# Performance work log

Measured on AMD Instinct MI355X. Metric: run time of the kernel, lower is better.

The kernel has to match this reference:

```python
import jax, jax.numpy as jnp
import numpy as np


def setup_inputs() -> dict:
    key = jax.random.key(0)
    k0, k1, k2, k3, k4 = jax.random.split(key, 5)
    B, N, H, d, kproj = 4, 2048, 8, 32, 256
    queries = jax.random.normal(k0, (B, N, H, d), dtype=jnp.float32)
    keys = jax.random.normal(k1, (B, N, H, d), dtype=jnp.float32)
    values = jax.random.normal(k2, (B, N, H, d), dtype=jnp.float32)
    # Linformer sequence projections [N, k]; scaled so projected K/V keep unit-ish variance
    E_proj = jax.random.normal(k3, (N, kproj), dtype=jnp.float32) * 0.02
    F_proj = jax.random.normal(k4, (N, kproj), dtype=jnp.float32) * 0.02
    return {"queries": queries, "keys": keys, "values": values,
            "E_proj": E_proj, "F_proj": F_proj}


def reference(queries, keys, values, E_proj, F_proj):
    """Hybrid attention of dsfa_former:
      (1) FullAttention with triangular causal mask (manual einsum+softmax)
      (2) LinearAttentionHead: Linformer-style sequence projection of K/V via E/F.
    Dropout is identity (eval). Returns (out_full, out_lin), each [B, N, H, d].
    """
    B, N, H, d = queries.shape
    scale = 1.0 / jnp.sqrt(jnp.asarray(d, queries.dtype))

    # ---- FullAttention (causal) ----
    scores = jnp.einsum('blhe,bshe->bhls', queries, keys)  # [B,H,N,N]
    causal = jnp.triu(jnp.ones((N, N), dtype=bool), k=1)   # True above diag -> masked
    scores = jnp.where(causal, -jnp.inf, scores)
    A = jax.nn.softmax(scale * scores, axis=-1)
    out_full = jnp.einsum('bhls,bshd->blhd', A, values)    # [B,N,H,d]

    # ---- LinearAttentionHead (Linformer, no causal mask since kp != N) ----
    Qb = queries.transpose(0, 2, 1, 3)  # [B,H,N,d]
    Kb = keys.transpose(0, 2, 1, 3)
    Vb = values.transpose(0, 2, 1, 3)
    Kp = jnp.einsum('bhnd,nk->bhkd', Kb, E_proj)           # [B,H,k,d]
    Vp = jnp.einsum('bhnd,nk->bhkd', Vb, F_proj)           # [B,H,k,d]
    s_lin = jnp.einsum('bhnd,bhkd->bhnk', Qb, Kp) * scale  # d_k == d
    P = jax.nn.softmax(s_lin, axis=-1)
    out_lin = jnp.einsum('bhnk,bhkd->bhnd', P, Vp).transpose(0, 2, 1, 3)  # [B,N,H,d]

    return out_full, out_lin
```

## Files before the change

kernel.cpp:

```cpp
#include <hip/hip_runtime.h>
#include <hip/hip_bf16.h>


typedef __bf16 bf16x8 __attribute__((ext_vector_type(8)));
typedef __bf16 bf16x2 __attribute__((ext_vector_type(2)));
typedef float f32x4 __attribute__((ext_vector_type(4)));

union BF8 { uint4 u4; ushort us[8]; bf16x8 b; unsigned u32[4]; };

constexpr int B_ = 4, N_ = 2048, H_ = 8, D_ = 32, KP_ = 256, BH_ = 32;
constexpr float SCL2 = 0.25505654442633533f;
constexpr int NFULL = 1024;
constexpr int CHK = 32 * D_;

__device__ __forceinline__ ushort f2bf(float f) {
  unsigned u = __builtin_bit_cast(unsigned, f);
  return (ushort)((u + 0x7FFFu + ((u >> 16) & 1u)) >> 16);
}
__device__ __forceinline__ unsigned pkbf(float f0, float f1) {
#if __has_builtin(__builtin_amdgcn_cvt_pk_bf16_f32)
  bf16x2 r = __builtin_amdgcn_cvt_pk_bf16_f32(f0, f1);
  return __builtin_bit_cast(unsigned, r);
#else
  unsigned u0 = __builtin_bit_cast(unsigned, f0) + 0x8000u;
  unsigned u1 = __builtin_bit_cast(unsigned, f1) + 0x8000u;
  return __builtin_amdgcn_perm(u1, u0, 0x07060302);
#endif
}
__device__ __forceinline__ float bflo(unsigned u) {
  return __builtin_bit_cast(float, u << 16);
}
__device__ __forceinline__ float bfhi(unsigned u) {
  return __builtin_bit_cast(float, u & 0xFFFF0000u);
}

__device__ __forceinline__ void load8_bf(const float* __restrict__ p,
                                         float scale, BF8& hi) {
  float4 a = *reinterpret_cast<const float4*>(p);
  float4 b = *reinterpret_cast<const float4*>(p + 4);
  float x[8] = {a.x, a.y, a.z, a.w, b.x, b.y, b.z, b.w};
#pragma unroll
  for (int i = 0; i < 8; ++i) hi.us[i] = f2bf(x[i] * scale);
}

__global__ __launch_bounds__(256) void k_prep(const float* __restrict__ K,
                                              const float* __restrict__ V,
                                              const float* __restrict__ E,
                                              const float* __restrict__ F,
                                              ushort* __restrict__ KH,
                                              ushort* __restrict__ Kt,
                                              ushort* __restrict__ Vt,
                                              ushort* __restrict__ Et,
                                              ushort* __restrict__ Ft) {
  __shared__ alignas(16) ushort S[4224];
  const int idx = blockIdx.x;
  const int t = threadIdx.x;
  if (idx < 1024) {
    ushort* Tk = S;
    ushort* Tv = S + 2112;
    const int bh = idx >> 5, b = bh >> 3, h = bh & 7;
    const int n0 = (idx & 31) * 64;
    {
      const int row = t >> 2, e8 = (t & 3) * 8;
      const size_t gbase = ((size_t)(b * N_ + n0 + row) * H_ + h) * D_ + e8;
      float4 k0 = *reinterpret_cast<const float4*>(K + gbase);
      float4 k1 = *reinterpret_cast<const float4*>(K + gbase + 4);
      float4 v0 = *reinterpret_cast<const float4*>(V + gbase);
      float4 v1 = *reinterpret_cast<const float4*>(V + gbase + 4);
      float kk[8] = {k0.x,k0.y,k0.z,k0.w,k1.x,k1.y,k1.z,k1.w};
      float vv[8] = {v0.x,v0.y,v0.z,v0.w,v1.x,v1.y,v1.z,v1.w};
      BF8 xh;
#pragma unroll
      for (int i = 0; i < 8; ++i) {
        xh.us[i] = f2bf(kk[i]);
        Tk[(e8 + i) * 66 + row] = xh.us[i];
        Tv[(e8 + i) * 66 + row] = f2bf(vv[i]);
      }
      *reinterpret_cast<uint4*>(KH + ((size_t)bh * N_ + n0 + row) * D_ + e8) = xh.u4;
    }
    __syncthreads();
    {
      const int e = t >> 3, n8 = (t & 7) * 8;
      BF8 xk, xv;
#pragma unroll
      for (int i = 0; i < 8; ++i) {
        xk.us[i] = Tk[e * 66 + n8 + i];
        xv.us[i] = Tv[e * 66 + n8 + i];
      }
      const size_t ob = ((size_t)bh * D_ + e) * N_ + n0 + n8;
      *reinterpret_cast<uint4*>(Kt + ob) = xk.u4;
      *reinterpret_cast<uint4*>(Vt + ob) = xv.u4;
    }
  } else {
    const int j = idx - 1024;
    const float* src = (j >> 7) ? F : E;
    ushort* dst = (j >> 7) ? Ft : Et;
    const int jj = j & 127;
    const int n0 = (jj & 31) * 64, kp0 = (jj >> 5) * 64;
    ushort* T = S;
    {
      const int n = t >> 2, c16 = (t & 3) * 16;
      const size_t gbase = (size_t)(n0 + n) * KP_ + kp0 + c16;
#pragma unroll
      for (int q = 0; q < 4; ++q) {
        float4 x = *reinterpret_cast<const float4*>(src + gbase + q * 4);
        T[(c16 + q * 4 + 0) * 66 + n] = f2bf(x.x);
        T[(c16 + q * 4 + 1) * 66 + n] = f2bf(x.y);
        T[(c16 + q * 4 + 2) * 66 + n] = f2bf(x.z);
        T[(c16 + q * 4 + 3) * 66 + n] = f2bf(x.w);
      }
    }
    __syncthreads();
    {
      const int kp = t >> 2, n16 = (t & 3) * 16;
      BF8 x0, x1;
#pragma unroll
      for (int i = 0; i < 8; ++i) {
        x0.us[i] = T[kp * 66 + n16 + i];
        x1.us[i] = T[kp * 66 + n16 + 8 + i];
      }
      const size_t ob = (size_t)(kp0 + kp) * N_ + n0 + n16;
      *reinterpret_cast<uint4*>(dst + ob) = x0.u4;
      *reinterpret_cast<uint4*>(dst + ob + 8) = x1.u4;
    }
  }
}

__global__ __launch_bounds__(256) void k_linproj(const ushort* __restrict__ Et,
                                                 const ushort* __restrict__ Ft,
                                                 const ushort* __restrict__ Kt,
                                                 const ushort* __restrict__ Vt,
                                                 ushort* __restrict__ Kp,
                                                 ushort* __restrict__ Vpt) {
  __shared__ float L[4][64][16];
  const int bh = blockIdx.y;
  const int t = threadIdx.x;
  const int w = t >> 6, lane = t & 63, quad = lane >> 4, l15 = lane & 15;
  const int kp16 = blockIdx.x * 16;
  const int nbase = w * (N_ / 4);

  const ushort* eA = Et + (size_t)(kp16 + l15) * N_ + nbase + quad * 8;
  const ushort* fA = Ft + (size_t)(kp16 + l15) * N_ + nbase + quad * 8;
  const ushort* kB0 = Kt + ((size_t)bh * D_ + l15) * N_ + nbase + quad * 8;
  const ushort* kB1 = kB0 + (size_t)16 * N_;
  const ushort* vB0 = Vt + ((size_t)bh * D_ + l15) * N_ + nbase + quad * 8;
  const ushort* vB1 = vB0 + (size_t)16 * N_;

  f32x4 accK0 = {0.f,0.f,0.f,0.f}, accK1 = {0.f,0.f,0.f,0.f};
  f32x4 accV0 = {0.f,0.f,0.f,0.f}, accV1 = {0.f,0.f,0.f,0.f};

  for (int n0 = 0; n0 < N_ / 4; n0 += 32) {
    BF8 aE, aF, b0, b1, b2, b3;
    aE.u4 = *reinterpret_cast<const uint4*>(eA + n0);
    aF.u4 = *reinterpret_cast<const uint4*>(fA + n0);
    b0.u4 = *reinterpret_cast<const uint4*>(kB0 + n0);
    b1.u4 = *reinterpret_cast<const uint4*>(kB1 + n0);
    b2.u4 = *reinterpret_cast<const uint4*>(vB0 + n0);
    b3.u4 = *reinterpret_cast<const uint4*>(vB1 + n0);
    accK0 = __builtin_amdgcn_mfma_f32_16x16x32_bf16(aE.b, b0.b, accK0, 0, 0, 0);
    accK1 = __builtin_amdgcn_mfma_f32_16x16x32_bf16(aE.b, b1.b, accK1, 0, 0, 0);
    accV0 = __builtin_amdgcn_mfma_f32_16x16x32_bf16(aF.b, b2.b, accV0, 0, 0, 0);
    accV1 = __builtin_amdgcn_mfma_f32_16x16x32_bf16(aF.b, b3.b, accV1, 0, 0, 0);
  }

#pragma unroll
  for (int r = 0; r < 4; ++r) {
    L[w][lane][r]      = accK0[r];
    L[w][lane][4 + r]  = accK1[r];
    L[w][lane][8 + r]  = accV0[r];
    L[w][lane][12 + r] = accV1[r];
  }
  __syncthreads();
#pragma unroll
  for (int r = 0; r < 4; ++r) {
    const float v = L[0][lane][w * 4 + r] + L[1][lane][w * 4 + r] +
                    L[2][lane][w * 4 + r] + L[3][lane][w * 4 + r];
    const int kp = kp16 + quad * 4 + r;
    if (w == 0)      Kp[((size_t)bh * KP_ + kp) * D_ + l15]       = f2bf(v);
    else if (w == 1) Kp[((size_t)bh * KP_ + kp) * D_ + 16 + l15]  = f2bf(v);
    else if (w == 2) Vpt[((size_t)bh * D_ + l15) * KP_ + kp]      = f2bf(v);
    else             Vpt[((size_t)bh * D_ + 16 + l15) * KP_ + kp] = f2bf(v);
  }
}

__global__ __launch_bounds__(256) void k_attn(const float* __restrict__ Q,
                                              const ushort* __restrict__ KH,
                                              const ushort* __restrict__ Vt,
                                              const ushort* __restrict__ Kp,
                                              const ushort* __restrict__ Vpt,
                                              float* __restrict__ out) {
  __shared__ unsigned Op[4][4][64][5];
  const int idx = blockIdx.x;
  const int t = threadIdx.x;
  const int w = t >> 6, lane = t & 63;
  const int quad = lane >> 4, l15 = lane & 15;
  const int kperm1 = 8 * (l15 >> 2) + (l15 & 3);
  const f32x4 z = {0.f,0.f,0.f,0.f};

  if (idx < NFULL) {
    const int bh = (idx & 7) + 8 * ((idx >> 3) & 3);
    const int m = 31 - (idx >> 5);
    const int b = bh >> 3, h = bh & 7;
    const int q0 = 64 * m;

    BF8 qh[4];
#pragma unroll
    for (int tt = 0; tt < 4; ++tt)
      load8_bf(Q + ((size_t)(b * N_ + q0 + 16 * tt + l15) * H_ + h) * D_ + quad * 8,
               SCL2, qh[tt]);

    const ushort* KHl = KH + (size_t)bh * N_ * D_ + (size_t)kperm1 * D_ + quad * 8;
    const ushort* V0l = Vt + ((size_t)bh * D_ + l15) * N_ + quad * 8;
    const ushort* V1l = V0l + (size_t)16 * N_;

    const int nun = 2 * m;
    const int cb = (w * nun) >> 2;
    const int ce = ((w + 1) * nun) >> 2;
    const int nwu = ce - cb;

    f32x4 O0[4], O1[4];
    float ls[4];
#pragma unroll
    for (int tt = 0; tt < 4; ++tt) { O0[tt] = z; O1[tt] = z; ls[tt] = 0.f; }

    BF8 kA1, kA2, vA0, vA1, kB1, kB2, vB0, vB1;

    auto procU = [&](BF8& k1, BF8& k2, BF8& v0, BF8& v1) {
#pragma unroll
      for (int tt = 0; tt < 4; ++tt) {
        f32x4 s1 = __builtin_amdgcn_mfma_f32_16x16x32_bf16(k1.b, qh[tt].b, z, 0, 0, 0);
        f32x4 s2 = __builtin_amdgcn_mfma_f32_16x16x32_bf16(k2.b, qh[tt].b, z, 0, 0, 0);
        float e0 = exp2f(s1[0]), e1 = exp2f(s1[1]), e2 = exp2f(s1[2]), e3 = exp2f(s1[3]);
        float e4 = exp2f(s2[0]), e5 = exp2f(s2[1]), e6 = exp2f(s2[2]), e7 = exp2f(s2[3]);
        ls[tt] += ((e0 + e1) + (e2 + e3)) + ((e4 + e5) + (e6 + e7));
        BF8 p;
        p.u32[0] = pkbf(e0, e1); p.u32[1] = pkbf(e2, e3);
        p.u32[2] = pkbf(e4, e5); p.u32[3] = pkbf(e6, e7);
        O0[tt] = __builtin_amdgcn_mfma_f32_16x16x32_bf16(p.b, v0.b, O0[tt], 0, 0, 0);
        O1[tt] = __builtin_amdgcn_mfma_f32_16x16x32_bf16(p.b, v1.b, O1[tt], 0, 0, 0);
      }
    };
    auto procM = [&](BF8& k1, BF8& k2, BF8& v0, BF8& v1, int ta, bool doUnm) {
#pragma unroll
      for (int d = 0; d < 2; ++d) {
        const int tt = ta + d;
        const int thr = d ? 16 + l15 : l15;
        f32x4 s1 = __builtin_amdgcn_mfma_f32_16x16x32_bf16(k1.b, qh[tt].b, z, 0, 0, 0);
        f32x4 s2 = __builtin_amdgcn_mfma_f32_16x16x32_bf16(k2.b, qh[tt].b, z, 0, 0, 0);
        float e[8];
#pragma unroll
        for (int j = 0; j < 8; ++j) {
          const float sv = (j < 4) ? s1[j] : s2[j - 4];
          e[j] = (8 * quad + j <= thr) ? exp2f(sv) : 0.f;
        }
        ls[tt] += ((e[0] + e[1]) + (e[2] + e[3])) + ((e[4] + e[5]) + (e[6] + e[7]));
        BF8 p;
        p.u32[0] = pkbf(e[0], e[1]); p.u32[1] = pkbf(e[2], e[3]);
        p.u32[2] = pkbf(e[4], e[5]); p.u32[3] = pkbf(e[6], e[7]);
        O0[tt] = __builtin_amdgcn_mfma_f32_16x16x32_bf16(p.b, v0.b, O0[tt], 0, 0, 0);
        O1[tt] = __builtin_amdgcn_mfma_f32_16x16x32_bf16(p.b, v1.b, O1[tt], 0, 0, 0);
      }
      if (doUnm) {
#pragma unroll
        for (int tt = 2; tt < 4; ++tt) {
          f32x4 s1 = __builtin_amdgcn_mfma_f32_16x16x32_bf16(k1.b, qh[tt].b, z, 0, 0, 0);
          f32x4 s2 = __builtin_amdgcn_mfma_f32_16x16x32_bf16(k2.b, qh[tt].b, z, 0, 0, 0);
          float e0 = exp2f(s1[0]), e1 = exp2f(s1[1]), e2 = exp2f(s1[2]), e3 = exp2f(s1[3]);
          float e4 = exp2f(s2[0]), e5 = exp2f(s2[1]), e6 = exp2f(s2[2]), e7 = exp2f(s2[3]);
          ls[tt] += ((e0 + e1) + (e2 + e3)) + ((e4 + e5) + (e6 + e7));
          BF8 p;
          p.u32[0] = pkbf(e0, e1); p.u32[1] = pkbf(e2, e3);
          p.u32[2] = pkbf(e4, e5); p.u32[3] = pkbf(e6, e7);
          O0[tt] = __builtin_amdgcn_mfma_f32_16x16x32_bf16(p.b, v0.b, O0[tt], 0, 0, 0);
          O1[tt] = __builtin_amdgcn_mfma_f32_16x16x32_bf16(p.b, v1.b, O1[tt], 0, 0, 0);
        }
      }
    };

    kA1.u4 = *reinterpret_cast<const uint4*>(KHl + (size_t)cb * CHK);
    kA2.u4 = *reinterpret_cast<const uint4*>(KHl + (size_t)cb * CHK + 4 * D_);
    vA0.u4 = *reinterpret_cast<const uint4*>(V0l + cb * 32);
    vA1.u4 = *reinterpret_cast<const uint4*>(V1l + cb * 32);
    kB1.u4 = *reinterpret_cast<const uint4*>(KHl + (size_t)(cb + 1) * CHK);
    kB2.u4 = *reinterpret_cast<const uint4*>(KHl + (size_t)(cb + 1) * CHK + 4 * D_);
    vB0.u4 = *reinterpret_cast<const uint4*>(V0l + (cb + 1) * 32);
    vB1.u4 = *reinterpret_cast<const uint4*>(V1l + (cb + 1) * 32);

    const ushort* pKA = KHl + (size_t)(cb + 2) * CHK;
    const ushort* pKB = KHl + (size_t)(cb + 3) * CHK;
    const ushort* pV0 = V0l + (cb + 2) * 32;
    const ushort* pV1 = V1l + (cb + 2) * 32;

    int i = 0;
    for (; i + 2 <= nwu; i += 2) {
      procU(kA1, kA2, vA0, vA1);
      kA1.u4 = *reinterpret_cast<const uint4*>(pKA);
      kA2.u4 = *reinterpret_cast<const uint4*>(pKA + 4 * D_);
      vA0.u4 = *reinterpret_cast<const uint4*>(pV0);
      vA1.u4 = *reinterpret_cast<const uint4*>(pV1);
      procU(kB1, kB2, vB0, vB1);
      kB1.u4 = *reinterpret_cast<const uint4*>(pKB);
      kB2.u4 = *reinterpret_cast<const uint4*>(pKB + 4 * D_);
      vB0.u4 = *reinterpret_cast<const uint4*>(pV0 + 32);
      vB1.u4 = *reinterpret_cast<const uint4*>(pV1 + 32);
      pKA += 2 * CHK; pKB += 2 * CHK; pV0 += 64; pV1 += 64;
    }
    if (i < nwu) {
      procU(kA1, kA2, vA0, vA1);
      if (w == 3) procM(kB1, kB2, vB0, vB1, 0, true);
    } else if (w == 3) {
      procM(kA1, kA2, vA0, vA1, 0, true);
    }
    if (w == 2) {
      const int c2 = nun + 1;
      kB1.u4 = *reinterpret_cast<const uint4*>(KHl + (size_t)c2 * CHK);
      kB2.u4 = *reinterpret_cast<const uint4*>(KHl + (size_t)c2 * CHK + 4 * D_);
      vB0.u4 = *reinterpret_cast<const uint4*>(V0l + c2 * 32);
      vB1.u4 = *reinterpret_cast<const uint4*>(V1l + c2 * 32);
      procM(kB1, kB2, vB0, vB1, 2, false);
    }

#pragma unroll
    for (int tt = 0; tt < 4; ++tt) {
      Op[w][tt][lane][0] = pkbf(O0[tt][0], O0[tt][1]);
      Op[w][tt][lane][1] = pkbf(O0[tt][2], O0[tt][3]);
      Op[w][tt][lane][2] = pkbf(O1[tt][0], O1[tt][1]);
      Op[w][tt][lane][3] = pkbf(O1[tt][2], O1[tt][3]);
      Op[w][tt][lane][4] = __builtin_bit_cast(unsigned, ls[tt]);
    }
    __syncthreads();
    {
      const int tt = w;
      float l = __builtin_bit_cast(float, Op[0][tt][lane][4]) +
                __builtin_bit_cast(float, Op[1][tt][lane][4]) +
                __builtin_bit_cast(float, Op[2][tt][lane][4]) +
                __builtin_bit_cast(float, Op[3][tt][lane][4]);
      l += __shfl_xor(l, 16);
      l += __shfl_xor(l, 32);
      const float inv = __builtin_amdgcn_rcpf(l);
      float A0[4] = {0.f,0.f,0.f,0.f}, A1[4] = {0.f,0.f,0.f,0.f};
#pragma unroll
      for (int s = 0; s < 4; ++s) {
        const unsigned u0 = Op[s][tt][lane][0], u1 = Op[s][tt][lane][1];
        const unsigned u2 = Op[s][tt][lane][2], u3 = Op[s][tt][lane][3];
        A0[0] += bflo(u0); A0[1] += bfhi(u0);
        A0[2] += bflo(u1); A0[3] += bfhi(u1);
        A1[0] += bflo(u2); A1[1] += bfhi(u2);
        A1[2] += bflo(u3); A1[3] += bfhi(u3);
      }
#pragma unroll
      for (int r = 0; r < 4; ++r) {
        const float fr = __shfl(inv, quad * 4 + r, 16);
        const int q = q0 + 16 * tt + quad * 4 + r;
        const size_t base = ((size_t)(b * N_ + q) * H_ + h) * D_;
        out[base + l15]      = A0[r] * fr;
        out[base + 16 + l15] = A1[r] * fr;
      }
    }
  } else {
    const int j = idx - NFULL;
    const int bh = (j & 7) + 8 * ((j >> 3) & 3);
    const int b = bh >> 3, h = bh & 7;
    const int q0 = (j >> 5) * 64 + w * 16;
    float* olin = out + (size_t)B_ * N_ * H_ * D_;

    BF8 qh;
    load8_bf(Q + ((size_t)(b * N_ + q0 + l15) * H_ + h) * D_ + quad * 8, SCL2, qh);

    const int kperm2 = kperm1 + 4;
    const ushort* KpHb = Kp + (size_t)bh * KP_ * D_ + quad * 8;
    const ushort* Vp0 = Vpt + ((size_t)bh * D_ + l15) * KP_ + quad * 8;
    const ushort* Vp1 = Vp0 + (size_t)16 * KP_;

    f32x4 s1[8], s2[8];
    float sum = 0.f;
#pragma unroll
    for (int g = 0; g < 8; ++g) {
      const int kp0 = g * 32;
      BF8 a1, a2;
      a1.u4 = *reinterpret_cast<const uint4*>(KpHb + (size_t)(kp0 + kperm1) * D_);
      a2.u4 = *reinterpret_cast<const uint4*>(KpHb + (size_t)(kp0 + kperm2) * D_);
      s1[g] = __builtin_amdgcn_mfma_f32_16x16x32_bf16(a1.b, qh.b, z, 0, 0, 0);
      s2[g] = __builtin_amdgcn_mfma_f32_16x16x32_bf16(a2.b, qh.b, z, 0, 0, 0);
#pragma unroll
      for (int r = 0; r < 4; ++r) {
        s1[g][r] = exp2f(s1[g][r]);
        s2[g][r] = exp2f(s2[g][r]);
        sum += s1[g][r] + s2[g][r];
      }
    }
    sum += __shfl_xor(sum, 16);
    sum += __shfl_xor(sum, 32);
    const float inv = __builtin_amdgcn_rcpf(sum);

    f32x4 O0 = z, O1 = z;
#pragma unroll
    for (int g = 0; g < 8; ++g) {
      BF8 p;
      p.u32[0] = pkbf(s1[g][0] * inv, s1[g][1] * inv);
      p.u32[1] = pkbf(s1[g][2] * inv, s1[g][3] * inv);
      p.u32[2] = pkbf(s2[g][0] * inv, s2[g][1] * inv);
      p.u32[3] = pkbf(s2[g][2] * inv, s2[g][3] * inv);
      BF8 v0, v1;
      v0.u4 = *reinterpret_cast<const uint4*>(Vp0 + g * 32);
      v1.u4 = *reinterpret_cast<const uint4*>(Vp1 + g * 32);
      O0 = __builtin_amdgcn_mfma_f32_16x16x32_bf16(p.b, v0.b, O0, 0, 0, 0);
      O1 = __builtin_amdgcn_mfma_f32_16x16x32_bf16(p.b, v1.b, O1, 0, 0, 0);
    }

#pragma unroll
    for (int r = 0; r < 4; ++r) {
      const int q = q0 + quad * 4 + r;
      const size_t base = ((size_t)(b * N_ + q) * H_ + h) * D_;
      olin[base + l15]      = O0[r];
      olin[base + 16 + l15] = O1[r];
    }
  }
}

extern "C" void kernel_launch(void* const* d_in, const int* in_sizes, int n_in,
                              void* d_out, int out_size, void* d_ws, size_t ws_size,
                              hipStream_t stream) {
  const float* Q = (const float*)d_in[0];
  const float* K = (const float*)d_in[1];
  const float* V = (const float*)d_in[2];
  const float* E = (const float*)d_in[3];
  const float* F = (const float*)d_in[4];
  float* out = (float*)d_out;

  ushort* KH  = (ushort*)d_ws;
  ushort* Kt  = KH + (size_t)BH_ * N_ * D_;
  ushort* Vt  = Kt + (size_t)BH_ * N_ * D_;
  ushort* Et  = Vt + (size_t)BH_ * N_ * D_;
  ushort* Ft  = Et + (size_t)KP_ * N_;
  ushort* Kp  = Ft + (size_t)KP_ * N_;
  ushort* Vpt = Kp + (size_t)BH_ * KP_ * D_;

  k_prep<<<dim3(1280), 256, 0, stream>>>(K, V, E, F, KH, Kt, Vt, Et, Ft);
  k_linproj<<<dim3(KP_ / 16, BH_), 256, 0, stream>>>(Et, Ft, Kt, Vt, Kp, Vpt);
  k_attn<<<dim3(NFULL + 1024), 256, 0, stream>>>(Q, KH, Vt, Kp, Vpt, out);
}
```

Measured before the change: 146.4 us.

## Compute softmax row sums via MFMA with ones vector and use raw exp2

Replaces per-lane VALU accumulation of exponentials with an extra MFMA against an all-ones bf16 operand, so row sums come out in the output layout and the shuffle reductions go away. Uses the hardware exp2 intrinsic instead of exp2f, adds an occupancy hint to launch bounds, and packs the shared-memory partial outputs into 16-byte vector stores with a separate small row-sum buffer. In the Linformer branch, normalisation moves after the PV product so unnormalised probabilities are packed once. This adds MFMA work per tile, and the row sums are now built from bf16-rounded probabilities.

```diff
diff --git a/kernel.cpp b/kernel.cpp
--- a/kernel.cpp
+++ b/kernel.cpp
@@ -32,6 +32,13 @@
 }
 __device__ __forceinline__ float bfhi(unsigned u) {
   return __builtin_bit_cast(float, u & 0xFFFF0000u);
+}
+__device__ __forceinline__ float ex2(float x) {
+#if __has_builtin(__builtin_amdgcn_exp2f)
+  return __builtin_amdgcn_exp2f(x);
+#else
+  return exp2f(x);
+#endif
 }
 
 __device__ __forceinline__ void load8_bf(const float* __restrict__ p,
@@ -183,13 +190,14 @@
   }
 }
 
-__global__ __launch_bounds__(256) void k_attn(const float* __restrict__ Q,
-                                              const ushort* __restrict__ KH,
-                                              const ushort* __restrict__ Vt,
-                                              const ushort* __restrict__ Kp,
-                                              const ushort* __restrict__ Vpt,
-                                              float* __restrict__ out) {
-  __shared__ unsigned Op[4][4][64][5];
+__global__ __launch_bounds__(256, 4) void k_attn(const float* __restrict__ Q,
+                                                 const ushort* __restrict__ KH,
+                                                 const ushort* __restrict__ Vt,
+                                                 const ushort* __restrict__ Kp,
+                                                 const ushort* __restrict__ Vpt,
+                                                 float* __restrict__ out) {
+  __shared__ alignas(16) unsigned Op[4][4][64][4];
+  __shared__ float Ls[4][4][4][4];
   const int idx = blockIdx.x;
   const int t = threadIdx.x;
   const int w = t >> 6, lane = t & 63;
@@ -197,6 +205,10 @@
   const int kperm1 = 8 * (l15 >> 2) + (l15 & 3);
   const f32x4 z = {0.f,0.f,0.f,0.f};
 
+  BF8 ones;
+#pragma unroll
+  for (int i2 = 0; i2 < 4; ++i2) ones.u32[i2] = 0x3F803F80u;
+
   if (idx < NFULL) {
     const int bh = (idx & 7) + 8 * ((idx >> 3) & 3);
     const int m = 31 - (idx >> 5);
@@ -218,10 +230,9 @@
     const int ce = ((w + 1) * nun) >> 2;
     const int nwu = ce - cb;
 
-    f32x4 O0[4], O1[4];
-    float ls[4];
-#pragma unroll
-    for (int tt = 0; tt < 4; ++tt) { O0[tt] = z; O1[tt] = z; ls[tt] = 0.f; }
+    f32x4 O0[4], O1[4], LS[4];
+#pragma unroll
+    for (int tt = 0; tt < 4; ++tt) { O0[tt] = z; O1[tt] = z; LS[tt] = z; }
 
     BF8 kA1, kA2, vA0, vA1, kB1, kB2, vB0, vB1;
 
@@ -230,14 +241,14 @@
       for (int tt = 0; tt < 4; ++tt) {
         f32x4 s1 = __builtin_amdgcn_mfma_f32_16x16x32_bf16(k1.b, qh[tt].b, z, 0, 0, 0);
         f32x4 s2 = __builtin_amdgcn_mfma_f32_16x16x32_bf16(k2.b, qh[tt].b, z, 0, 0, 0);
-        float e0 = exp2f(s1[0]), e1 = exp2f(s1[1]), e2 = exp2f(s1[2]), e3 = exp2f(s1[3]);
-        float e4 = exp2f(s2[0]), e5 = exp2f(s2[1]), e6 = exp2f(s2[2]), e7 = exp2f(s2[3]);
-        ls[tt] += ((e0 + e1) + (e2 + e3)) + ((e4 + e5) + (e6 + e7));
+        float e0 = ex2(s1[0]), e1 = ex2(s1[1]), e2 = ex2(s1[2]), e3 = ex2(s1[3]);
+        float e4 = ex2(s2[0]), e5 = ex2(s2[1]), e6 = ex2(s2[2]), e7 = ex2(s2[3]);
         BF8 p;
         p.u32[0] = pkbf(e0, e1); p.u32[1] = pkbf(e2, e3);
         p.u32[2] = pkbf(e4, e5); p.u32[3] = pkbf(e6, e7);
         O0[tt] = __builtin_amdgcn_mfma_f32_16x16x32_bf16(p.b, v0.b, O0[tt], 0, 0, 0);
         O1[tt] = __builtin_amdgcn_mfma_f32_16x16x32_bf16(p.b, v1.b, O1[tt], 0, 0, 0);
+        LS[tt] = __builtin_amdgcn_mfma_f32_16x16x32_bf16(p.b, ones.b, LS[tt], 0, 0, 0);
       }
     };
     auto procM = [&](BF8& k1, BF8& k2, BF8& v0, BF8& v1, int ta, bool doUnm) {
@@ -251,28 +262,28 @@
 #pragma unroll
         for (int j = 0; j < 8; ++j) {
           const float sv = (j < 4) ? s1[j] : s2[j - 4];
-          e[j] = (8 * quad + j <= thr) ? exp2f(sv) : 0.f;
+          e[j] = (8 * quad + j <= thr) ? ex2(sv) : 0.f;
         }
-        ls[tt] += ((e[0] + e[1]) + (e[2] + e[3])) + ((e[4] + e[5]) + (e[6] + e[7]));
         BF8 p;
         p.u32[0] = pkbf(e[0], e[1]); p.u32[1] = pkbf(e[2], e[3]);
         p.u32[2] = pkbf(e[4], e[5]); p.u32[3] = pkbf(e[6], e[7]);
         O0[tt] = __builtin_amdgcn_mfma_f32_16x16x32_bf16(p.b, v0.b, O0[tt], 0, 0, 0);
         O1[tt] = __builtin_amdgcn_mfma_f32_16x16x32_bf16(p.b, v1.b, O1[tt], 0, 0, 0);
+        LS[tt] = __builtin_amdgcn_mfma_f32_16x16x32_bf16(p.b, ones.b, LS[tt], 0, 0, 0);
       }
       if (doUnm) {
 #pragma unroll
         for (int tt = 2; tt < 4; ++tt) {
           f32x4 s1 = __builtin_amdgcn_mfma_f32_16x16x32_bf16(k1.b, qh[tt].b, z, 0, 0, 0);
           f32x4 s2 = __builtin_amdgcn_mfma_f32_16x16x32_bf16(k2.b, qh[tt].b, z, 0, 0, 0);
-          float e0 = exp2f(s1[0]), e1 = exp2f(s1[1]), e2 = exp2f(s1[2]), e3 = exp2f(s1[3]);
-          float e4 = exp2f(s2[0]), e5 = exp2f(s2[1]), e6 = exp2f(s2[2]), e7 = exp2f(s2[3]);
-          ls[tt] += ((e0 + e1) + (e2 + e3)) + ((e4 + e5) + (e6 + e7));
+          float e0 = ex2(s1[0]), e1 = ex2(s1[1]), e2 = ex2(s1[2]), e3 = ex2(s1[3]);
+          float e4 = ex2(s2[0]), e5 = ex2(s2[1]), e6 = ex2(s2[2]), e7 = ex2(s2[3]);
           BF8 p;
           p.u32[0] = pkbf(e0, e1); p.u32[1] = pkbf(e2, e3);
           p.u32[2] = pkbf(e4, e5); p.u32[3] = pkbf(e6, e7);
           O0[tt] = __builtin_amdgcn_mfma_f32_16x16x32_bf16(p.b, v0.b, O0[tt], 0, 0, 0);
           O1[tt] = __builtin_amdgcn_mfma_f32_16x16x32_bf16(p.b, v1.b, O1[tt], 0, 0, 0);
+          LS[tt] = __builtin_amdgcn_mfma_f32_16x16x32_bf16(p.b, ones.b, LS[tt], 0, 0, 0);
         }
       }
     };
@@ -322,39 +333,44 @@
 
 #pragma unroll
     for (int tt = 0; tt < 4; ++tt) {
-      Op[w][tt][lane][0] = pkbf(O0[tt][0], O0[tt][1]);
-      Op[w][tt][lane][1] = pkbf(O0[tt][2], O0[tt][3]);
-      Op[w][tt][lane][2] = pkbf(O1[tt][0], O1[tt][1]);
-      Op[w][tt][lane][3] = pkbf(O1[tt][2], O1[tt][3]);
-      Op[w][tt][lane][4] = __builtin_bit_cast(unsigned, ls[tt]);
+      uint4 pk;
+      pk.x = pkbf(O0[tt][0], O0[tt][1]);
+      pk.y = pkbf(O0[tt][2], O0[tt][3]);
+      pk.z = pkbf(O1[tt][0], O1[tt][1]);
+      pk.w = pkbf(O1[tt][2], O1[tt][3]);
+      *reinterpret_cast<uint4*>(Op[w][tt][lane]) = pk;
+    }
+    if (l15 == 0) {
+#pragma unroll
+      for (int tt = 0; tt < 4; ++tt)
+#pragma unroll
+        for (int r = 0; r < 4; ++r) Ls[w][tt][quad][r] = LS[tt][r];
     }
     __syncthreads();
     {
       const int tt = w;
-      float l = __builtin_bit_cast(float, Op[0][tt][lane][4]) +
-                __builtin_bit_cast(float, Op[1][tt][lane][4]) +
-                __builtin_bit_cast(float, Op[2][tt][lane][4]) +
-                __builtin_bit_cast(float, Op[3][tt][lane][4]);
-      l += __shfl_xor(l, 16);
-      l += __shfl_xor(l, 32);
-      const float inv = __builtin_amdgcn_rcpf(l);
+      float iv[4];
+#pragma unroll
+      for (int r = 0; r < 4; ++r) {
+        const float l = Ls[0][tt][quad][r] + Ls[1][tt][quad][r] +
+                        Ls[2][tt][quad][r] + Ls[3][tt][quad][r];
+        iv[r] = __builtin_amdgcn_rcpf(l);
+      }
       float A0[4] = {0.f,0.f,0.f,0.f}, A1[4] = {0.f,0.f,0.f,0.f};
 #pragma unroll
       for (int s = 0; s < 4; ++s) {
-        const unsigned u0 = Op[s][tt][lane][0], u1 = Op[s][tt][lane][1];
-        const unsigned u2 = Op[s][tt][lane][2], u3 = Op[s][tt][lane][3];
-        A0[0] += bflo(u0); A0[1] += bfhi(u0);
-        A0[2] += bflo(u1); A0[3] += bfhi(u1);
-        A1[0] += bflo(u2); A1[1] += bfhi(u2);
-        A1[2] += bflo(u3); A1[3] += bfhi(u3);
+        const uint4 u = *reinterpret_cast<const uint4*>(Op[s][tt][lane]);
+        A0[0] += bflo(u.x); A0[1] += bfhi(u.x);
+        A0[2] += bflo(u.y); A0[3] += bfhi(u.y);
+        A1[0] += bflo(u.z); A1[1] += bfhi(u.z);
+        A1[2] += bflo(u.w); A1[3] += bfhi(u.w);
       }
 #pragma unroll
       for (int r = 0; r < 4; ++r) {
-        const float fr = __shfl(inv, quad * 4 + r, 16);
         const int q = q0 + 16 * tt + quad * 4 + r;
         const size_t base = ((size_t)(b * N_ + q) * H_ + h) * D_;
-        out[base + l15]      = A0[r] * fr;
-        out[base + 16 + l15] = A1[r] * fr;
+        out[base + l15]      = A0[r] * iv[r];
+        out[base + 16 + l15] = A1[r] * iv[r];
       }
     }
   } else {
@@ -372,48 +388,40 @@
     const ushort* Vp0 = Vpt + ((size_t)bh * D_ + l15) * KP_ + quad * 8;
     const ushort* Vp1 = Vp0 + (size_t)16 * KP_;
 
-    f32x4 s1[8], s2[8];
-    float sum = 0.f;
+    BF8 pg[8];
+    f32x4 LSum = z;
 #pragma unroll
     for (int g = 0; g < 8; ++g) {
       const int kp0 = g * 32;
       BF8 a1, a2;
       a1.u4 = *reinterpret_cast<const uint4*>(KpHb + (size_t)(kp0 + kperm1) * D_);
       a2.u4 = *reinterpret_cast<const uint4*>(KpHb + (size_t)(kp0 + kperm2) * D_);
-      s1[g] = __builtin_amdgcn_mfma_f32_16x16x32_bf16(a1.b, qh.b, z, 0, 0, 0);
-      s2[g] = __builtin_amdgcn_mfma_f32_16x16x32_bf16(a2.b, qh.b, z, 0, 0, 0);
-#pragma unroll
-      for (int r = 0; r < 4; ++r) {
-        s1[g][r] = exp2f(s1[g][r]);
-        s2[g][r] = exp2f(s2[g][r]);
-        sum += s1[g][r] + s2[g][r];
-      }
-    }
-    sum += __shfl_xor(sum, 16);
-    sum += __shfl_xor(sum, 32);
-    const float inv = __builtin_amdgcn_rcpf(sum);
+      f32x4 s1 = __builtin_amdgcn_mfma_f32_16x16x32_bf16(a1.b, qh.b, z, 0, 0, 0);
+      f32x4 s2 = __builtin_amdgcn_mfma_f32_16x16x32_bf16(a2.b, qh.b, z, 0, 0, 0);
+      const float e0 = ex2(s1[0]), e1 = ex2(s1[1]), e2 = ex2(s1[2]), e3 = ex2(s1[3]);
+      const float e4 = ex2(s2[0]), e5 = ex2(s2[1]), e6 = ex2(s2[2]), e7 = ex2(s2[3]);
+      pg[g].u32[0] = pkbf(e0, e1); pg[g].u32[1] = pkbf(e2, e3);
+      pg[g].u32[2] = pkbf(e4, e5); pg[g].u32[3] = pkbf(e6, e7);
+      LSum = __builtin_amdgcn_mfma_f32_16x16x32_bf16(pg[g].b, ones.b, LSum, 0, 0, 0);
+    }
 
     f32x4 O0 = z, O1 = z;
 #pragma unroll
     for (int g = 0; g < 8; ++g) {
-      BF8 p;
-      p.u32[0] = pkbf(s1[g][0] * inv, s1[g][1] * inv);
-      p.u32[1] = pkbf(s1[g][2] * inv, s1[g][3] * inv);
-      p.u32[2] = pkbf(s2[g][0] * inv, s2[g][1] * inv);
-      p.u32[3] = pkbf(s2[g][2] * inv, s2[g][3] * inv);
       BF8 v0, v1;
       v0.u4 = *reinterpret_cast<const uint4*>(Vp0 + g * 32);
       v1.u4 = *reinterpret_cast<const uint4*>(Vp1 + g * 32);
-      O0 = __builtin_amdgcn_mfma_f32_16x16x32_bf16(p.b, v0.b, O0, 0, 0, 0);
-      O1 = __builtin_amdgcn_mfma_f32_16x16x32_bf16(p.b, v1.b, O1, 0, 0, 0);
+      O0 = __builtin_amdgcn_mfma_f32_16x16x32_bf16(pg[g].b, v0.b, O0, 0, 0, 0);
+      O1 = __builtin_amdgcn_mfma_f32_16x16x32_bf16(pg[g].b, v1.b, O1, 0, 0, 0);
     }
 
 #pragma unroll
     for (int r = 0; r < 4; ++r) {
+      const float fr = __builtin_amdgcn_rcpf(LSum[r]);
       const int q = q0 + quad * 4 + r;
       const size_t base = ((size_t)(b * N_ + q) * H_ + h) * D_;
-      olin[base + l15]      = O0[r];
-      olin[base + 16 + l15] = O1[r];
+      olin[base + l15]      = O0[r] * fr;
+      olin[base + 16 + l15] = O1[r] * fr;
     }
   }
 }
```

Result: faster. 142.0 us (-3.0%).
